# Performance work log

Hardware: AMD Instinct MI355X
Metric: run time of the kernel (lower is better)

Reference implementation:

```python
import jax, jax.numpy as jnp
import numpy as np

B, T, N_EMBED, HEAD_SIZE = 8, 2048, 1024, 64


def setup_inputs() -> dict:
    key = jax.random.key(0)
    kx, kq, kk, kv = jax.random.split(key, 4)
    x = jax.random.normal(kx, (B, T, N_EMBED), dtype=jnp.float32)
    # nn.Linear(n_embed, head_size, bias=False) -> weight [head_size, n_embed];
    # we store the transposed [n_embed, head_size] so projection is x @ W.
    s = 1.0 / np.sqrt(N_EMBED)
    Wq = jax.random.normal(kq, (N_EMBED, HEAD_SIZE), dtype=jnp.float32) * s
    Wk = jax.random.normal(kk, (N_EMBED, HEAD_SIZE), dtype=jnp.float32) * s
    Wv = jax.random.normal(kv, (N_EMBED, HEAD_SIZE), dtype=jnp.float32) * s
    pad_mask = jnp.ones((B, T), dtype=jnp.int32)
    return {"x": x, "pad_mask": pad_mask, "Wq": Wq, "Wk": Wk, "Wv": Wv}


def reference(x, pad_mask, Wq, Wk, Wv):
    Bq, Tq, C = x.shape  # C == n_embed
    q = x @ Wq  # [B,T,H]
    k = x @ Wk  # self-attention path (enc_x is None)
    v = x @ Wv
    # NOTE: original divides by C**0.5 with C = n_embed, not head_size.
    scores = jnp.einsum("bth,bsh->bts", q, k) / jnp.sqrt(jnp.asarray(C, x.dtype))
    causal = jnp.tril(jnp.ones((Tq, Tq), dtype=bool))  # tril[:T,:T] != 0
    keep = causal[None, :, :] & (pad_mask[:, None, :] != 0)  # [B,T,T]
    scores = jnp.where(keep, scores, -jnp.inf)
    attn = jax.nn.softmax(scores, axis=-1)
    return jnp.einsum("bts,bsh->bth", attn, v)  # [B,T,head_size]
```

## Files before the change

### kernel.cpp

```cpp
#include <hip/hip_runtime.h>

#define DEV static __device__ __forceinline__

typedef float f32x4 __attribute__((ext_vector_type(4)));
typedef int i32x4 __attribute__((ext_vector_type(4)));
typedef __bf16 bf16x8 __attribute__((ext_vector_type(8)));
typedef unsigned short u16x8 __attribute__((ext_vector_type(8)));
typedef unsigned short u16x4 __attribute__((ext_vector_type(4)));

#define MFMA(a, b, c) __builtin_amdgcn_mfma_f32_16x16x32_bf16((a), (b), (c), 0, 0, 0)

#define WAIT5_BARRIER() asm volatile("s_waitcnt vmcnt(5)\n\ts_barrier" ::: "memory")
#define VM0_BARRIER()   asm volatile("s_waitcnt vmcnt(0)\n\ts_barrier" ::: "memory")
#define LGKM_BARRIER()  asm volatile("s_waitcnt lgkmcnt(0)\n\ts_barrier" ::: "memory")
#define VM_DRAIN()      asm volatile("s_waitcnt vmcnt(0)" ::: "memory")

#define TT 2048
#define CE 1024
#define HS 64

#define WBT_E 0
#define Q_E   196608
#define K_E   (Q_E + 1048576)
#define VT_E  (K_E + 1048576)
#define PO_E  (VT_E + 1048576)
#define PML_E (PO_E + 4718592)

DEV unsigned short cvt_bf16(float f) {
    unsigned int u = __builtin_bit_cast(unsigned int, f);
    u += 0x7FFFu + ((u >> 16) & 1u);
    return (unsigned short)(u >> 16);
}

DEV float bf2f(unsigned short v) {
    unsigned int u = ((unsigned int)v) << 16;
    return __builtin_bit_cast(float, u);
}

DEV bf16x8 ld_bf8(const unsigned short* p) {
    union { u16x8 u; bf16x8 b; } v;
    v.u = *(const u16x8*)p;
    return v.b;
}

DEV bf16x8 as_bf8(u16x8 u) {
    union { u16x8 u; bf16x8 b; } v;
    v.u = u;
    return v.b;
}

DEV void glds16(const void* g, void* l) {
    __builtin_amdgcn_global_load_lds(
        (const __attribute__((address_space(1))) void*)g,
        (__attribute__((address_space(3))) void*)l, 16, 0, 0);
}

__global__ __launch_bounds__(256) void wconv_kernel(
        const float* __restrict__ Wq, const float* __restrict__ Wk,
        const float* __restrict__ Wv, unsigned short* __restrict__ wbt) {
    __shared__ unsigned short Tr[64 * 72];
    const int blk = blockIdx.x;
    const int head = blk >> 4, kt = blk & 15;
    const int k0 = kt * 64;
    const float* W = (head == 0) ? Wq : ((head == 1) ? Wk : Wv);
    const float sc = (head == 0) ? 0.045084220027780106f : 1.0f;
    const int t = threadIdx.x;
    const int rrow = t >> 4, c4 = (t & 15) * 4;
    for (int i = 0; i < 4; ++i) {
        int krow = rrow + i * 16;
        f32x4 f = *(const f32x4*)(W + (size_t)(k0 + krow) * 64 + c4);
        Tr[(c4 + 0) * 72 + krow] = cvt_bf16(f[0] * sc);
        Tr[(c4 + 1) * 72 + krow] = cvt_bf16(f[1] * sc);
        Tr[(c4 + 2) * 72 + krow] = cvt_bf16(f[2] * sc);
        Tr[(c4 + 3) * 72 + krow] = cvt_bf16(f[3] * sc);
    }
    __syncthreads();
    const int n = t >> 2, off = (t & 3) * 16;
    u16x8 a0 = *(const u16x8*)&Tr[n * 72 + off];
    u16x8 a1 = *(const u16x8*)&Tr[n * 72 + off + 8];
    unsigned short* dst = wbt + head * 65536 + n * 1024 + k0 + off;
    *(u16x8*)dst = a0;
    *(u16x8*)(dst + 8) = a1;
}

__global__ __launch_bounds__(512, 2) void proj_kernel(
        const float* __restrict__ x, const unsigned short* __restrict__ wbt,
        unsigned short* __restrict__ qws, unsigned short* __restrict__ kws,
        unsigned short* __restrict__ vtws) {
    __shared__ __align__(16) float Xt0[4096], Xt1[4096], Xt2[4096];
    __shared__ __align__(16) unsigned short Wt0[12288], Wt1[12288], Wt2[12288];
    __shared__ __align__(16) unsigned short TT2[64 * 72];

    const int t = threadIdx.x;
    const int lane = t & 63, w = t >> 6;
    const int quad = lane >> 4, c = lane & 15;
    const int wm = w & 1, wn = w >> 1;
    const int t0 = blockIdx.x * 64;
    const int ck7 = c & 7;

    const int sxr = lane >> 4;
    const int sxc0 = (lane & 15) ^ sxr;
    const int sxc1 = (lane & 15) ^ ((4 + sxr) & 7);
    const float* xg0 = x + (size_t)(t0 + w * 8 + 0 + sxr) * CE + sxc0 * 4;
    const float* xg1 = x + (size_t)(t0 + w * 8 + 4 + sxr) * CE + sxc1 * 4;
    const int swc = lane >> 3;
    const int swk = (lane & 7) ^ swc;
    const unsigned short* wg0 = wbt + (size_t)(w * 24 + 0 + swc) * 1024 + swk * 8;
    const unsigned short* wg1 = wbt + (size_t)(w * 24 + 8 + swc) * 1024 + swk * 8;
    const unsigned short* wg2 = wbt + (size_t)(w * 24 + 16 + swc) * 1024 + swk * 8;

#define PSTAGE(XD, WD, ks) { \
    const int kf = (ks) * 64; \
    glds16(xg0 + kf, &XD[(w * 8 + 0) * 64]); \
    glds16(xg1 + kf, &XD[(w * 8 + 4) * 64]); \
    glds16(wg0 + kf, &WD[(w * 24 + 0) * 64]); \
    glds16(wg1 + kf, &WD[(w * 24 + 8) * 64]); \
    glds16(wg2 + kf, &WD[(w * 24 + 16) * 64]); }

    f32x4 acc[2][3] = {};

    PSTAGE(Xt0, Wt0, 0)
    PSTAGE(Xt1, Wt1, 1)

#define PITER(step, XT, WT, XD, WD) { \
    WAIT5_BARRIER(); \
    bf16x8 af[2][2]; \
    _Pragma("unroll") for (int rf = 0; rf < 2; ++rf) \
    _Pragma("unroll") for (int kk = 0; kk < 2; ++kk) { \
        const int row = wm * 32 + rf * 16 + c; \
        const int lc = kk * 8 + quad * 2; \
        f32x4 v0 = *(const f32x4*)&XT[row * 64 + ((lc ^ ck7) * 4)]; \
        f32x4 v1 = *(const f32x4*)&XT[row * 64 + (((lc + 1) ^ ck7) * 4)]; \
        u16x8 ap; \
        _Pragma("unroll") for (int j = 0; j < 4; ++j) { \
            ap[j] = cvt_bf16(v0[j]); ap[4 + j] = cvt_bf16(v1[j]); } \
        af[rf][kk] = as_bf8(ap); \
    } \
    _Pragma("unroll") for (int nt = 0; nt < 3; ++nt) \
    _Pragma("unroll") for (int kk = 0; kk < 2; ++kk) { \
        const int col = wn * 48 + nt * 16 + c; \
        bf16x8 bb = ld_bf8(&WT[col * 64 + (((kk * 4 + quad) ^ ck7) * 8)]); \
        acc[0][nt] = MFMA(af[0][kk], bb, acc[0][nt]); \
        acc[1][nt] = MFMA(af[1][kk], bb, acc[1][nt]); \
    } \
    PSTAGE(XD, WD, (((step) + 2) & 15)) }

    for (int s = 0; s < 15; s += 3) {
        PITER(s + 0, Xt0, Wt0, Xt2, Wt2)
        PITER(s + 1, Xt1, Wt1, Xt0, Wt0)
        PITER(s + 2, Xt2, Wt2, Xt1, Wt1)
    }
    PITER(15, Xt0, Wt0, Xt2, Wt2)
#undef PITER
#undef PSTAGE

#pragma unroll
    for (int rf = 0; rf < 2; ++rf) {
#pragma unroll
        for (int nt = 0; nt < 3; ++nt) {
            int col = wn * 48 + nt * 16 + c;
            f32x4 a = acc[rf][nt];
#pragma unroll
            for (int r4 = 0; r4 < 4; ++r4) {
                int row = wm * 32 + rf * 16 + quad * 4 + r4;
                size_t tg = (size_t)(t0 + row);
                unsigned short hv = cvt_bf16(a[r4]);
                if (col < 64)       qws[tg * HS + col] = hv;
                else if (col < 128) kws[tg * HS + col - 64] = hv;
                else                TT2[(col - 128) * 72 + row] = hv;
            }
        }
    }
    __syncthreads();
    {
        int h = t >> 3, off = (t & 7) * 8;
        u16x8 v = *(const u16x8*)&TT2[h * 72 + off];
        int b = t0 >> 11, tl0 = t0 & 2047;
        *(u16x8*)(vtws + (size_t)(b * 64 + h) * TT + tl0 + off) = v;
    }
}

__global__ __launch_bounds__(256) void flash_kernel(
        const unsigned short* __restrict__ qws, const unsigned short* __restrict__ kws,
        const unsigned short* __restrict__ vtws, const int* __restrict__ pmask,
        unsigned short* __restrict__ pO, float* __restrict__ pml) {
    __shared__ __align__(16) unsigned short Kt0[4096], Kt1[4096];
    __shared__ __align__(16) unsigned short Vt0[4096], Vt1[4096];
    __shared__ __align__(16) unsigned short Ps[4][1152];
    __shared__ __align__(16) float Bs[256];

    const int t = threadIdx.x, blk = blockIdx.x;
    const int b = blk / 144, cid = blk - b * 144;
    int g = 0;
    while (cid >= 2 * (g + 1) * (g + 2)) ++g;
    const int off = cid - 2 * g * (g + 1);
    const int qi = off / (g + 1);
    const int chunk = off - qi * (g + 1);
    const int qt = 4 * g + qi;
    const int jbeg = chunk * 4;
    int je = jbeg + 4; if (je > qt + 1) je = qt + 1;
    const int jend = je;
    const int niter = jend - jbeg;

    const int lane = t & 63, w = t >> 6;
    const int quad = lane >> 4, c = lane & 15;

    const int srow = lane >> 3, scb = (lane & 7) ^ srow;
    const unsigned short* kg0 = kws + (size_t)(b * TT + 2 * w * 8 + srow) * HS + scb * 8;
    const unsigned short* kg1 = kg0 + (size_t)8 * HS;
    const unsigned short* vg0 = vtws + (size_t)(b * 64 + 2 * w * 8 + srow) * TT + scb * 8;
    const unsigned short* vg1 = vg0 + (size_t)8 * TT;

#define FSTAGE(KD, VD, kv) \
    glds16(kg0 + (size_t)(kv) * HS, &KD[(2 * w + 0) * 512]); \
    glds16(kg1 + (size_t)(kv) * HS, &KD[(2 * w + 1) * 512]); \
    glds16(vg0 + (kv), &VD[(2 * w + 0) * 512]); \
    glds16(vg1 + (kv), &VD[(2 * w + 1) * 512]);

    bf16x8 qf[2];
#pragma unroll
    for (int kk = 0; kk < 2; ++kk)
        qf[kk] = ld_bf8(qws + (size_t)(b * TT + qt * 64 + w * 16 + c) * HS + kk * 32 + quad * 8);

    {
        int bi = t * 4;
        if (bi < niter * 64) {
            i32x4 pmv = *(const i32x4*)(pmask + b * TT + jbeg * 64 + bi);
            f32x4 bvv;
#pragma unroll
            for (int j = 0; j < 4; ++j) bvv[j] = pmv[j] ? 0.0f : -1e30f;
            *(f32x4*)&Bs[bi] = bvv;
        }
    }

    FSTAGE(Kt0, Vt0, jbeg * 64)
    LGKM_BARRIER();

    f32x4 o[4] = {};
    float m_run = -1e30f, l_run = 0.0f;
    const int ck7 = c & 7;

#define FITER(u, KT, VT, KD, VD) \
    if (j0 + (u) < jend) { \
        const int j = j0 + (u); \
        VM0_BARRIER(); \
        { int jn = j + 1; if (jn > jend - 1) jn = jend - 1; \
          FSTAGE(KD, VD, jn * 64) } \
        f32x4 bv[4]; \
        _Pragma("unroll") for (int nt = 0; nt < 4; ++nt) \
            bv[nt] = *(const f32x4*)&Bs[(j - jbeg) * 64 + nt * 16 + quad * 4]; \
        f32x4 s4[4] = {}; \
        _Pragma("unroll") for (int kk = 0; kk < 2; ++kk) \
        _Pragma("unroll") for (int nt = 0; nt < 4; ++nt) { \
            bf16x8 ka = ld_bf8(&KT[(nt * 16 + c) * 64 + (((kk * 4 + quad) ^ ck7) * 8)]); \
            s4[nt] = MFMA(ka, qf[kk], s4[nt]); } \
        if (j == qt) { \
            const int qrl = w * 16 + c; \
            _Pragma("unroll") for (int nt = 0; nt < 4; ++nt) \
            _Pragma("unroll") for (int r = 0; r < 4; ++r) { \
                int kvl = nt * 16 + quad * 4 + r; \
                s4[nt][r] = (kvl > qrl) ? -1e30f : (s4[nt][r] + bv[nt][r]); } \
        } else { \
            _Pragma("unroll") for (int nt = 0; nt < 4; ++nt) \
            _Pragma("unroll") for (int r = 0; r < 4; ++r) s4[nt][r] += bv[nt][r]; } \
        float mx = s4[0][0]; \
        _Pragma("unroll") for (int nt = 0; nt < 4; ++nt) \
        _Pragma("unroll") for (int r = 0; r < 4; ++r) mx = fmaxf(mx, s4[nt][r]); \
        mx = fmaxf(mx, __shfl_xor(mx, 16, 64)); \
        mx = fmaxf(mx, __shfl_xor(mx, 32, 64)); \
        float mnew = fmaxf(m_run, mx); \
        float al = exp2f(m_run - mnew); \
        m_run = mnew; \
        _Pragma("unroll") for (int nt = 0; nt < 4; ++nt) \
        _Pragma("unroll") for (int r = 0; r < 4; ++r) s4[nt][r] = exp2f(s4[nt][r] - mnew); \
        float rs = 0.0f; \
        _Pragma("unroll") for (int nt = 0; nt < 4; ++nt) \
            rs += (s4[nt][0] + s4[nt][1]) + (s4[nt][2] + s4[nt][3]); \
        rs += __shfl_xor(rs, 16, 64); \
        rs += __shfl_xor(rs, 32, 64); \
        l_run = l_run * al + rs; \
        _Pragma("unroll") for (int ht = 0; ht < 4; ++ht) \
        _Pragma("unroll") for (int r = 0; r < 4; ++r) o[ht][r] *= al; \
        _Pragma("unroll") for (int nt = 0; nt < 4; ++nt) { \
            u16x4 pk; \
            _Pragma("unroll") for (int r = 0; r < 4; ++r) pk[r] = cvt_bf16(s4[nt][r]); \
            *(u16x4*)&Ps[w][c * 72 + nt * 16 + quad * 4] = pk; } \
        bf16x8 p0 = ld_bf8(&Ps[w][c * 72 + quad * 8]); \
        bf16x8 p1 = ld_bf8(&Ps[w][c * 72 + 32 + quad * 8]); \
        _Pragma("unroll") for (int kk = 0; kk < 2; ++kk) { \
            bf16x8 pa = kk ? p1 : p0; \
            _Pragma("unroll") for (int ht = 0; ht < 4; ++ht) { \
                bf16x8 va = ld_bf8(&VT[(ht * 16 + c) * 64 + (((kk * 4 + quad) ^ ck7) * 8)]); \
                o[ht] = MFMA(va, pa, o[ht]); } } \
    }

    for (int j0 = jbeg; j0 < jend; j0 += 2) {
        FITER(0, Kt0, Vt0, Kt1, Vt1)
        FITER(1, Kt1, Vt1, Kt0, Vt0)
    }
#undef FITER
#undef FSTAGE

    VM_DRAIN();

    unsigned short* po = pO + (size_t)blk * 4096;
#pragma unroll
    for (int ht = 0; ht < 4; ++ht) {
        u16x4 pk;
#pragma unroll
        for (int r = 0; r < 4; ++r) pk[r] = cvt_bf16(o[ht][r]);
        *(u16x4*)(po + (w * 16 + c) * 64 + ht * 16 + quad * 4) = pk;
    }
    if (quad == 0) {
        pml[(size_t)blk * 128 + (w * 16 + c) * 2] = m_run;
        pml[(size_t)blk * 128 + (w * 16 + c) * 2 + 1] = l_run;
    }
}

__global__ __launch_bounds__(256) void combine_kernel(
        const unsigned short* __restrict__ pO, const float* __restrict__ pml,
        float* __restrict__ out) {
    const int gid = blockIdx.x * 256 + threadIdx.x;
    const int h = gid & 63;
    const int grow = gid >> 6;
    const int b = grow >> 11;
    const int rin = grow & 2047;
    const int qt = rin >> 6;
    const int row = rin & 63;
    const int g = qt >> 2;
    const int nc = g + 1;
    const int s0 = b * 144 + 2 * g * (g + 1) + (qt - 4 * g) * (g + 1);

    float m_[8], l_[8], o_[8];
#pragma unroll
    for (int s = 0; s < 8; ++s) {
        const int slot = s0 + (s < nc ? s : 0);
        const float2 ml = *(const float2*)(pml + (size_t)slot * 128 + row * 2);
        const float ov = bf2f(pO[(size_t)slot * 4096 + row * 64 + h]);
        m_[s] = (s < nc) ? ml.x : -3.0e38f;
        l_[s] = (s < nc) ? ml.y : 0.0f;
        o_[s] = (s < nc) ? ov : 0.0f;
    }
    float M = m_[0];
#pragma unroll
    for (int s = 1; s < 8; ++s) M = fmaxf(M, m_[s]);
    float num = 0.0f, den = 0.0f;
#pragma unroll
    for (int s = 0; s < 8; ++s) {
        const float ww = exp2f(m_[s] - M);
        num += o_[s] * ww;
        den += l_[s] * ww;
    }
    out[(size_t)(b * TT + qt * 64 + row) * HS + h] = num / den;
}

extern "C" void kernel_launch(void* const* d_in, const int* in_sizes, int n_in,
                              void* d_out, int out_size, void* d_ws, size_t ws_size,
                              hipStream_t stream) {
    const float* x  = (const float*)d_in[0];
    const int* pm   = (const int*)d_in[1];
    const float* Wq = (const float*)d_in[2];
    const float* Wk = (const float*)d_in[3];
    const float* Wv = (const float*)d_in[4];
    float* out = (float*)d_out;

    unsigned short* wsu  = (unsigned short*)d_ws;
    unsigned short* wbt  = wsu + WBT_E;
    unsigned short* qws  = wsu + Q_E;
    unsigned short* kws  = wsu + K_E;
    unsigned short* vtws = wsu + VT_E;
    unsigned short* pO   = wsu + PO_E;
    float* pml           = (float*)(wsu + PML_E);

    wconv_kernel<<<48, 256, 0, stream>>>(Wq, Wk, Wv, wbt);
    proj_kernel<<<256, 512, 0, stream>>>(x, wbt, qws, kws, vtws);
    flash_kernel<<<1152, 256, 0, stream>>>(qws, kws, vtws, pm, pO, pml);
    combine_kernel<<<4096, 256, 0, stream>>>(pO, pml, out);
}
```

Baseline: 139.9 us.

## Fuse split-KV combine into flash kernel via last-block atomic counter

Removes the separate combine kernel launch. Each flash block now increments a per-query-tile atomic counter after writing its partial output and softmax stats, and the last block to finish for that tile merges all partials and writes the final output. The counters are reset inside the projection kernel so no extra launch is needed. This saves a launch and a full pass over the partials, at the cost of thread fences, an atomic, and a serial 16-row merge loop run by only the last-arriving block.

```diff
diff --git a/kernel.cpp b/kernel.cpp
--- a/kernel.cpp
+++ b/kernel.cpp
@@ -25,6 +25,7 @@
 #define VT_E  (K_E + 1048576)
 #define PO_E  (VT_E + 1048576)
 #define PML_E (PO_E + 4718592)
+#define CNT_E (PML_E + 294912)
 
 DEV unsigned short cvt_bf16(float f) {
     unsigned int u = __builtin_bit_cast(unsigned int, f);
@@ -86,12 +87,13 @@
 __global__ __launch_bounds__(512, 2) void proj_kernel(
         const float* __restrict__ x, const unsigned short* __restrict__ wbt,
         unsigned short* __restrict__ qws, unsigned short* __restrict__ kws,
-        unsigned short* __restrict__ vtws) {
+        unsigned short* __restrict__ vtws, int* __restrict__ cnt) {
     __shared__ __align__(16) float Xt0[4096], Xt1[4096], Xt2[4096];
     __shared__ __align__(16) unsigned short Wt0[12288], Wt1[12288], Wt2[12288];
     __shared__ __align__(16) unsigned short TT2[64 * 72];
 
     const int t = threadIdx.x;
+    if (t == 0) cnt[blockIdx.x] = 0;
     const int lane = t & 63, w = t >> 6;
     const int quad = lane >> 4, c = lane & 15;
     const int wm = w & 1, wn = w >> 1;
@@ -183,11 +185,13 @@
 __global__ __launch_bounds__(256) void flash_kernel(
         const unsigned short* __restrict__ qws, const unsigned short* __restrict__ kws,
         const unsigned short* __restrict__ vtws, const int* __restrict__ pmask,
-        unsigned short* __restrict__ pO, float* __restrict__ pml) {
+        unsigned short* __restrict__ pO, float* __restrict__ pml,
+        int* __restrict__ cnt, float* __restrict__ out) {
     __shared__ __align__(16) unsigned short Kt0[4096], Kt1[4096];
     __shared__ __align__(16) unsigned short Vt0[4096], Vt1[4096];
     __shared__ __align__(16) unsigned short Ps[4][1152];
     __shared__ __align__(16) float Bs[256];
+    __shared__ int lastf;
 
     const int t = threadIdx.x, blk = blockIdx.x;
     const int b = blk / 144, cid = blk - b * 144;
@@ -315,43 +319,43 @@
         pml[(size_t)blk * 128 + (w * 16 + c) * 2] = m_run;
         pml[(size_t)blk * 128 + (w * 16 + c) * 2 + 1] = l_run;
     }
-}
-
-__global__ __launch_bounds__(256) void combine_kernel(
-        const unsigned short* __restrict__ pO, const float* __restrict__ pml,
-        float* __restrict__ out) {
-    const int gid = blockIdx.x * 256 + threadIdx.x;
-    const int h = gid & 63;
-    const int grow = gid >> 6;
-    const int b = grow >> 11;
-    const int rin = grow & 2047;
-    const int qt = rin >> 6;
-    const int row = rin & 63;
-    const int g = qt >> 2;
+
+    __threadfence();
+    if (t == 0) {
+        int old = atomicAdd(cnt + (b * 32 + qt), 1);
+        lastf = (old == g);
+    }
+    __syncthreads();
+    if (!lastf) return;
+    __threadfence();
+
     const int nc = g + 1;
     const int s0 = b * 144 + 2 * g * (g + 1) + (qt - 4 * g) * (g + 1);
-
-    float m_[8], l_[8], o_[8];
-#pragma unroll
-    for (int s = 0; s < 8; ++s) {
-        const int slot = s0 + (s < nc ? s : 0);
-        const float2 ml = *(const float2*)(pml + (size_t)slot * 128 + row * 2);
-        const float ov = bf2f(pO[(size_t)slot * 4096 + row * 64 + h]);
-        m_[s] = (s < nc) ? ml.x : -3.0e38f;
-        l_[s] = (s < nc) ? ml.y : 0.0f;
-        o_[s] = (s < nc) ? ov : 0.0f;
-    }
-    float M = m_[0];
-#pragma unroll
-    for (int s = 1; s < 8; ++s) M = fmaxf(M, m_[s]);
-    float num = 0.0f, den = 0.0f;
-#pragma unroll
-    for (int s = 0; s < 8; ++s) {
-        const float ww = exp2f(m_[s] - M);
-        num += o_[s] * ww;
-        den += l_[s] * ww;
-    }
-    out[(size_t)(b * TT + qt * 64 + row) * HS + h] = num / den;
+    const int h = t & 63, rg0 = t >> 6;
+    for (int i = 0; i < 16; ++i) {
+        const int row = rg0 + i * 4;
+        float m_[8], l_[8], o_[8];
+#pragma unroll
+        for (int s = 0; s < 8; ++s) {
+            const int slot = s0 + (s < nc ? s : 0);
+            const float2 ml = *(const float2*)(pml + (size_t)slot * 128 + row * 2);
+            const float ov = bf2f(pO[(size_t)slot * 4096 + row * 64 + h]);
+            m_[s] = (s < nc) ? ml.x : -3.0e38f;
+            l_[s] = (s < nc) ? ml.y : 0.0f;
+            o_[s] = (s < nc) ? ov : 0.0f;
+        }
+        float M = m_[0];
+#pragma unroll
+        for (int s = 1; s < 8; ++s) M = fmaxf(M, m_[s]);
+        float num = 0.0f, den = 0.0f;
+#pragma unroll
+        for (int s = 0; s < 8; ++s) {
+            const float ww = exp2f(m_[s] - M);
+            num += o_[s] * ww;
+            den += l_[s] * ww;
+        }
+        out[(size_t)(b * TT + qt * 64 + row) * HS + h] = num / den;
+    }
 }
 
 extern "C" void kernel_launch(void* const* d_in, const int* in_sizes, int n_in,
@@ -371,9 +375,9 @@
     unsigned short* vtws = wsu + VT_E;
     unsigned short* pO   = wsu + PO_E;
     float* pml           = (float*)(wsu + PML_E);
+    int* cnt             = (int*)(wsu + CNT_E);
 
     wconv_kernel<<<48, 256, 0, stream>>>(Wq, Wk, Wv, wbt);
-    proj_kernel<<<256, 512, 0, stream>>>(x, wbt, qws, kws, vtws);
-    flash_kernel<<<1152, 256, 0, stream>>>(qws, kws, vtws, pm, pO, pml);
-    combine_kernel<<<4096, 256, 0, stream>>>(pO, pml, out);
-}
+    proj_kernel<<<256, 512, 0, stream>>>(x, wbt, qws, kws, vtws, cnt);
+    flash_kernel<<<1152, 256, 0, stream>>>(qws, kws, vtws, pm, pO, pml, cnt, out);
+}
```

Result: slower. 346.7 us (+147.9%).

## Stage x through registers and convert to bf16 once before LDS in projection

Applied to the files above, without the earlier changes.

The projection kernel no longer copies fp32 x tiles straight into LDS with async global-to-LDS loads. Each thread now loads its slice of x into registers two steps ahead, converts it to bf16 once, and writes a padded bf16 tile, so every wave reads ready bf16 fragments instead of repeating the fp32-to-bf16 conversion. This cuts x LDS footprint and the redundant conversion work. In exchange it adds register pressure and a different wait-count scheme, and launch bounds drop to one block per CU-slot hint.

```diff
diff --git a/kernel.cpp b/kernel.cpp
--- a/kernel.cpp
+++ b/kernel.cpp
@@ -10,7 +10,7 @@
 
 #define MFMA(a, b, c) __builtin_amdgcn_mfma_f32_16x16x32_bf16((a), (b), (c), 0, 0, 0)
 
-#define WAIT5_BARRIER() asm volatile("s_waitcnt vmcnt(5)\n\ts_barrier" ::: "memory")
+#define PBAR()          asm volatile("s_waitcnt vmcnt(3) lgkmcnt(0)\n\ts_barrier" ::: "memory")
 #define VM0_BARRIER()   asm volatile("s_waitcnt vmcnt(0)\n\ts_barrier" ::: "memory")
 #define LGKM_BARRIER()  asm volatile("s_waitcnt lgkmcnt(0)\n\ts_barrier" ::: "memory")
 #define VM_DRAIN()      asm volatile("s_waitcnt vmcnt(0)" ::: "memory")
@@ -83,11 +83,11 @@
     *(u16x8*)(dst + 8) = a1;
 }
 
-__global__ __launch_bounds__(512, 2) void proj_kernel(
+__global__ __launch_bounds__(512, 1) void proj_kernel(
         const float* __restrict__ x, const unsigned short* __restrict__ wbt,
         unsigned short* __restrict__ qws, unsigned short* __restrict__ kws,
         unsigned short* __restrict__ vtws) {
-    __shared__ __align__(16) float Xt0[4096], Xt1[4096], Xt2[4096];
+    __shared__ __align__(16) unsigned short Xt0[64 * 72], Xt1[64 * 72];
     __shared__ __align__(16) unsigned short Wt0[12288], Wt1[12288], Wt2[12288];
     __shared__ __align__(16) unsigned short TT2[64 * 72];
 
@@ -98,61 +98,71 @@
     const int t0 = blockIdx.x * 64;
     const int ck7 = c & 7;
 
-    const int sxr = lane >> 4;
-    const int sxc0 = (lane & 15) ^ sxr;
-    const int sxc1 = (lane & 15) ^ ((4 + sxr) & 7);
-    const float* xg0 = x + (size_t)(t0 + w * 8 + 0 + sxr) * CE + sxc0 * 4;
-    const float* xg1 = x + (size_t)(t0 + w * 8 + 4 + sxr) * CE + sxc1 * 4;
+    const int xr = t >> 3, xc = t & 7;
+    const float* xg = x + (size_t)(t0 + xr) * CE + xc * 8;
     const int swc = lane >> 3;
     const int swk = (lane & 7) ^ swc;
     const unsigned short* wg0 = wbt + (size_t)(w * 24 + 0 + swc) * 1024 + swk * 8;
     const unsigned short* wg1 = wbt + (size_t)(w * 24 + 8 + swc) * 1024 + swk * 8;
     const unsigned short* wg2 = wbt + (size_t)(w * 24 + 16 + swc) * 1024 + swk * 8;
 
-#define PSTAGE(XD, WD, ks) { \
+#define WSTAGE(WD, ks) { \
     const int kf = (ks) * 64; \
-    glds16(xg0 + kf, &XD[(w * 8 + 0) * 64]); \
-    glds16(xg1 + kf, &XD[(w * 8 + 4) * 64]); \
     glds16(wg0 + kf, &WD[(w * 24 + 0) * 64]); \
     glds16(wg1 + kf, &WD[(w * 24 + 8) * 64]); \
     glds16(wg2 + kf, &WD[(w * 24 + 16) * 64]); }
 
     f32x4 acc[2][3] = {};
-
-    PSTAGE(Xt0, Wt0, 0)
-    PSTAGE(Xt1, Wt1, 1)
-
-#define PITER(step, XT, WT, XD, WD) { \
-    WAIT5_BARRIER(); \
+    f32x4 xA0, xA1, xB0, xB1;
+
+    f32x4 p0 = *(const f32x4*)(xg);
+    f32x4 p1 = *(const f32x4*)(xg + 4);
+    xA0 = *(const f32x4*)(xg + 64);
+    xA1 = *(const f32x4*)(xg + 68);
+    WSTAGE(Wt0, 0)
+    WSTAGE(Wt1, 1)
+    {
+        u16x8 xp;
+#pragma unroll
+        for (int j = 0; j < 4; ++j) { xp[j] = cvt_bf16(p0[j]); xp[4 + j] = cvt_bf16(p1[j]); }
+        *(u16x8*)&Xt0[xr * 72 + xc * 8] = xp;
+    }
+
+#define PITER(step, WT, WD, XT, XD, RL0, RL1, RC0, RC1) { \
+    PBAR(); \
+    { const int kn = ((step) + 2 > 15 ? 15 : (step) + 2) * 64; \
+      RL0 = *(const f32x4*)(xg + kn); \
+      RL1 = *(const f32x4*)(xg + kn + 4); } \
     bf16x8 af[2][2]; \
     _Pragma("unroll") for (int rf = 0; rf < 2; ++rf) \
-    _Pragma("unroll") for (int kk = 0; kk < 2; ++kk) { \
-        const int row = wm * 32 + rf * 16 + c; \
-        const int lc = kk * 8 + quad * 2; \
-        f32x4 v0 = *(const f32x4*)&XT[row * 64 + ((lc ^ ck7) * 4)]; \
-        f32x4 v1 = *(const f32x4*)&XT[row * 64 + (((lc + 1) ^ ck7) * 4)]; \
-        u16x8 ap; \
-        _Pragma("unroll") for (int j = 0; j < 4; ++j) { \
-            ap[j] = cvt_bf16(v0[j]); ap[4 + j] = cvt_bf16(v1[j]); } \
-        af[rf][kk] = as_bf8(ap); \
-    } \
+    _Pragma("unroll") for (int kk = 0; kk < 2; ++kk) \
+        af[rf][kk] = ld_bf8(&XT[(wm * 32 + rf * 16 + c) * 72 + (kk * 4 + quad) * 8]); \
     _Pragma("unroll") for (int nt = 0; nt < 3; ++nt) \
     _Pragma("unroll") for (int kk = 0; kk < 2; ++kk) { \
         const int col = wn * 48 + nt * 16 + c; \
         bf16x8 bb = ld_bf8(&WT[col * 64 + (((kk * 4 + quad) ^ ck7) * 8)]); \
         acc[0][nt] = MFMA(af[0][kk], bb, acc[0][nt]); \
-        acc[1][nt] = MFMA(af[1][kk], bb, acc[1][nt]); \
-    } \
-    PSTAGE(XD, WD, (((step) + 2) & 15)) }
-
-    for (int s = 0; s < 15; s += 3) {
-        PITER(s + 0, Xt0, Wt0, Xt2, Wt2)
-        PITER(s + 1, Xt1, Wt1, Xt0, Wt0)
-        PITER(s + 2, Xt2, Wt2, Xt1, Wt1)
-    }
-    PITER(15, Xt0, Wt0, Xt2, Wt2)
+        acc[1][nt] = MFMA(af[1][kk], bb, acc[1][nt]); } \
+    { u16x8 xp; \
+      _Pragma("unroll") for (int j = 0; j < 4; ++j) { \
+          xp[j] = cvt_bf16(RC0[j]); xp[4 + j] = cvt_bf16(RC1[j]); } \
+      *(u16x8*)&XD[xr * 72 + xc * 8] = xp; } \
+    WSTAGE(WD, ((step) + 2 > 15 ? 15 : (step) + 2)) }
+
+    for (int s = 0; s < 12; s += 6) {
+        PITER(s + 0, Wt0, Wt2, Xt0, Xt1, xB0, xB1, xA0, xA1)
+        PITER(s + 1, Wt1, Wt0, Xt1, Xt0, xA0, xA1, xB0, xB1)
+        PITER(s + 2, Wt2, Wt1, Xt0, Xt1, xB0, xB1, xA0, xA1)
+        PITER(s + 3, Wt0, Wt2, Xt1, Xt0, xA0, xA1, xB0, xB1)
+        PITER(s + 4, Wt1, Wt0, Xt0, Xt1, xB0, xB1, xA0, xA1)
+        PITER(s + 5, Wt2, Wt1, Xt1, Xt0, xA0, xA1, xB0, xB1)
+    }
+    PITER(12, Wt0, Wt2, Xt0, Xt1, xB0, xB1, xA0, xA1)
+    PITER(13, Wt1, Wt0, Xt1, Xt0, xA0, xA1, xB0, xB1)
+    PITER(14, Wt2, Wt1, Xt0, Xt1, xB0, xB1, xA0, xA1)
+    PITER(15, Wt0, Wt2, Xt1, Xt0, xA0, xA1, xB0, xB1)
 #undef PITER
-#undef PSTAGE
+#undef WSTAGE
 
 #pragma unroll
     for (int rf = 0; rf < 2; ++rf) {
```

New measurement: 142.5 us. No clear change (+1.9%).
